# Performance work log

Measured on AMD Instinct MI355X. Metric: run time of the kernel, lower is better.

Reference implementation:

```python
import jax, jax.numpy as jnp
import numpy as np

EMBED_DIM = 768
NUM_HEADS = 12
HEAD_DIM = EMBED_DIM // NUM_HEADS
B, L = 1, 2048


def setup_inputs() -> dict:
    key = jax.random.key(0)
    ks = jax.random.split(key, 10)
    D = EMBED_DIM
    s = 1.0 / np.sqrt(D)
    x = jax.random.normal(ks[0], (B, L, D), dtype=jnp.float32)
    Wq = jax.random.uniform(ks[1], (D, D), jnp.float32, -s, s)
    bq = jax.random.uniform(ks[2], (D,), jnp.float32, -s, s)
    Wk = jax.random.uniform(ks[3], (D, D), jnp.float32, -s, s)
    bk = jax.random.uniform(ks[4], (D,), jnp.float32, -s, s)
    Wv = jax.random.uniform(ks[5], (D, D), jnp.float32, -s, s)
    bv = jax.random.uniform(ks[6], (D,), jnp.float32, -s, s)
    Wo = jax.random.uniform(ks[7], (D, D), jnp.float32, -s, s)
    bo = jax.random.uniform(ks[8], (D,), jnp.float32, -s, s)
    theta = jnp.zeros((1, NUM_HEADS, 1, 1), dtype=jnp.float32)
    return {"x": x, "Wq": Wq, "bq": bq, "Wk": Wk, "bk": bk,
            "Wv": Wv, "bv": bv, "Wo": Wo, "bo": bo, "theta": theta}


def _heads(t):
    # [B,L,D] -> [B,H,L,d_k]
    b, l, d = t.shape
    return t.reshape(b, l, NUM_HEADS, HEAD_DIM).transpose(0, 2, 1, 3)


def reference(x, Wq, bq, Wk, bk, Wv, bv, Wo, bo, theta):
    b, l, d = x.shape
    d_k = HEAD_DIM
    q = _heads(x @ Wq.T + bq)  # [B,H,L,dk]
    k = _heads(x @ Wk.T + bk)
    v = _heads(x @ Wv.T + bv)
    # squared pairwise L2 distance (== torch.cdist(q,k,p=2)**2), scaled by d_k
    qn = jnp.sum(q * q, axis=-1, keepdims=True)          # [B,H,L,1]
    kn = jnp.sum(k * k, axis=-1, keepdims=True)          # [B,H,L,1]
    qk = jnp.einsum('bhid,bhjd->bhij', q, k)             # [B,H,L,L]
    dist_sq = jnp.maximum(qn + kn.transpose(0, 1, 3, 2) - 2.0 * qk, 0.0) / d_k
    # global max over the full LxL matrix per (B,H)
    dist_max = jnp.max(dist_sq, axis=(-1, -2), keepdims=True)
    dist_norm = dist_sq / (dist_max + 1e-6)
    dsexp = jnp.exp(theta)                               # [1,H,1,1]
    attn_logits = jnp.exp(-dsexp * dist_norm)            # [B,H,L,L]
    attn_weights = jax.nn.softmax(attn_logits, axis=-1)
    context = jnp.einsum('bhij,bhjd->bhid', attn_weights, v)  # [B,H,L,dk]
    context = context.transpose(0, 2, 1, 3).reshape(b, l, d)
    output = context @ Wo.T + bo
    return output, attn_weights.mean(axis=1)
```

## Files before the change

kernel.cpp:

```cpp
#include <hip/hip_runtime.h>
#include <hip/hip_bf16.h>


typedef __bf16 bf16_t;
typedef bf16_t bf16x8 __attribute__((ext_vector_type(8)));
typedef bf16_t bf16x4 __attribute__((ext_vector_type(4)));
typedef float f32x4 __attribute__((ext_vector_type(4)));

#define L_SEQ 2048
#define DIM 768
#define NH 12
#define DKH 64
#define MDJ 8

__device__ __forceinline__ bf16x8 ldg8(const bf16_t* p) { return *(const bf16x8*)p; }
__device__ __forceinline__ f32x4 mfma16(bf16x8 a, bf16x8 b, f32x4 c_) {
  return __builtin_amdgcn_mfma_f32_16x16x32_bf16(a, b, c_, 0, 0, 0);
}


struct Tile2 { bf16x8 r[2]; };

__device__ __forceinline__ void tile_load(const bf16_t* __restrict__ src, int stride,
                                          Tile2& t_, int tid) {
#pragma unroll
  for (int c = 0; c < 2; ++c) {
    int chunk = tid + c * 256;
    t_.r[c] = *(const bf16x8*)&src[(size_t)(chunk >> 3) * stride + (chunk & 7) * 8];
  }
}

__device__ __forceinline__ void tile_write(bf16_t (*dst)[72], const Tile2& t_, int tid) {
#pragma unroll
  for (int c = 0; c < 2; ++c) {
    int chunk = tid + c * 256;
    *(bf16x8*)&dst[chunk >> 3][(chunk & 7) * 8] = t_.r[c];
  }
}

__device__ __forceinline__ void mfma_nt64(bf16_t (*As)[72], bf16_t (*Bs)[72],
                                          int wid, int lane, f32x4 acc[4]) {
#pragma unroll
  for (int ks = 0; ks < 2; ++ks) {
    bf16x8 a = *(const bf16x8*)&As[wid * 16 + (lane & 15)][ks * 32 + (lane >> 4) * 8];
#pragma unroll
    for (int nt = 0; nt < 4; ++nt) {
      bf16x8 b = *(const bf16x8*)&Bs[nt * 16 + (lane & 15)][ks * 32 + (lane >> 4) * 8];
      acc[nt] = mfma16(a, b, acc[nt]);
    }
  }
}


__global__ void cast_x(const float* __restrict__ in, bf16_t* __restrict__ out, int n4) {
  int i = blockIdx.x * 256 + threadIdx.x;
  if (i >= n4) return;
  float4 v = ((const float4*)in)[i];
  bf16_t* o = out + (size_t)i * 4;
  o[0] = (bf16_t)v.x; o[1] = (bf16_t)v.y; o[2] = (bf16_t)v.z; o[3] = (bf16_t)v.w;
}

__global__ void cast_w4(const float* __restrict__ w0, const float* __restrict__ w1,
                        const float* __restrict__ w2, const float* __restrict__ w3,
                        bf16_t* __restrict__ o0, bf16_t* __restrict__ o1,
                        bf16_t* __restrict__ o2, bf16_t* __restrict__ o3, int n4) {
  int i = blockIdx.x * 256 + threadIdx.x;
  if (i >= n4) return;
  const float* in = blockIdx.y == 0 ? w0 : blockIdx.y == 1 ? w1 : blockIdx.y == 2 ? w2 : w3;
  bf16_t* out = blockIdx.y == 0 ? o0 : blockIdx.y == 1 ? o1 : blockIdx.y == 2 ? o2 : o3;
  float4 v = ((const float4*)in)[i];
  bf16_t* o = out + (size_t)i * 4;
  o[0] = (bf16_t)v.x; o[1] = (bf16_t)v.y; o[2] = (bf16_t)v.z; o[3] = (bf16_t)v.w;
}


__global__ __launch_bounds__(256) void gemm_qkv(const bf16_t* __restrict__ x,
                                                const bf16_t* __restrict__ Bq,
                                                const bf16_t* __restrict__ Bk,
                                                const bf16_t* __restrict__ Bv,
                                                const float* __restrict__ bq,
                                                const float* __restrict__ bk,
                                                const float* __restrict__ bv,
                                                bf16_t* __restrict__ qo,
                                                bf16_t* __restrict__ ko,
                                                bf16_t* __restrict__ vto,
                                                float* __restrict__ qn,
                                                float* __restrict__ kn) {
  __shared__ bf16_t As[2][64][72];
  __shared__ bf16_t Bs[2][64][72];
  const int z = blockIdx.z;
  const bf16_t* B = z == 0 ? Bq : z == 1 ? Bk : Bv;
  const float* bias = z == 0 ? bq : z == 1 ? bk : bv;
  const int tid = threadIdx.x, wid = tid >> 6, lane = tid & 63;
  const int c = lane & 15, hi = lane >> 4;
  const int m0 = blockIdx.y * 64, n0 = blockIdx.x * 64;
  Tile2 at, bt;
  tile_load(x + (size_t)m0 * DIM, DIM, at, tid);
  tile_load(B + (size_t)n0 * DIM, DIM, bt, tid);
  f32x4 acc[4] = {};
  for (int kk = 0; kk < 12; ++kk) {
    tile_write(As[kk & 1], at, tid);
    tile_write(Bs[kk & 1], bt, tid);
    __syncthreads();
    if (kk < 11) {
      tile_load(x + (size_t)m0 * DIM + (kk + 1) * 64, DIM, at, tid);
      tile_load(B + (size_t)n0 * DIM + (kk + 1) * 64, DIM, bt, tid);
    }
    mfma_nt64(As[kk & 1], Bs[kk & 1], wid, lane, acc);
    __syncthreads();
  }
  const int r0 = wid * 16 + hi * 4;
  float ss[4] = {0.f, 0.f, 0.f, 0.f};
#pragma unroll
  for (int nt = 0; nt < 4; ++nt) {
    int cc = n0 + nt * 16 + c;
    float bv_ = bias[cc];
    int h = cc >> 6, d = cc & 63;
#pragma unroll
    for (int r = 0; r < 4; ++r) {
      int mm = m0 + r0 + r;
      float val = acc[nt][r] + bv_;
      if (z == 2) {
        vto[(size_t)cc * L_SEQ + mm] = (bf16_t)val;
      } else {
        bf16_t* out = z == 0 ? qo : ko;
        out[((size_t)h * L_SEQ + mm) * 64 + d] = (bf16_t)val;
        ss[r] = fmaf(val, val, ss[r]);
      }
    }
  }
  if (z < 2) {
#pragma unroll
    for (int s = 1; s < 16; s <<= 1)
#pragma unroll
      for (int r = 0; r < 4; ++r) ss[r] += __shfl_xor(ss[r], s);
    if (c == 0) {
      float* norm = z == 0 ? qn : kn;
      int h = n0 >> 6;
#pragma unroll
      for (int r = 0; r < 4; ++r) norm[h * L_SEQ + m0 + r0 + r] = ss[r];
    }
  }
}

__global__ __launch_bounds__(256) void gemm_out(const bf16_t* __restrict__ A,
                                                const bf16_t* __restrict__ B,
                                                const float* __restrict__ bias,
                                                float* __restrict__ out) {
  __shared__ bf16_t As[2][64][72];
  __shared__ bf16_t Bs[2][64][72];
  const int tid = threadIdx.x, wid = tid >> 6, lane = tid & 63;
  const int c = lane & 15, hi = lane >> 4;
  const int m0 = blockIdx.y * 64, n0 = blockIdx.x * 64;
  Tile2 at, bt;
  tile_load(A + (size_t)m0 * DIM, DIM, at, tid);
  tile_load(B + (size_t)n0 * DIM, DIM, bt, tid);
  f32x4 acc[4] = {};
  for (int kk = 0; kk < 12; ++kk) {
    tile_write(As[kk & 1], at, tid);
    tile_write(Bs[kk & 1], bt, tid);
    __syncthreads();
    if (kk < 11) {
      tile_load(A + (size_t)m0 * DIM + (kk + 1) * 64, DIM, at, tid);
      tile_load(B + (size_t)n0 * DIM + (kk + 1) * 64, DIM, bt, tid);
    }
    mfma_nt64(As[kk & 1], Bs[kk & 1], wid, lane, acc);
    __syncthreads();
  }
  const int r0 = wid * 16 + hi * 4;
#pragma unroll
  for (int nt = 0; nt < 4; ++nt) {
    int cc = n0 + nt * 16 + c;
    float bv = bias[cc];
#pragma unroll
    for (int r = 0; r < 4; ++r)
      out[(size_t)(m0 + r0 + r) * DIM + cc] = acc[nt][r] + bv;
  }
}


__global__ __launch_bounds__(256) void maxdist(const bf16_t* __restrict__ q,
                                               const bf16_t* __restrict__ k,
                                               const float* __restrict__ qn,
                                               const float* __restrict__ kn,
                                               float* __restrict__ blockmax) {
  __shared__ bf16_t Ks[2][64][72];
  __shared__ float wmax[4];
  const int it = blockIdx.x, jc = blockIdx.y, h = blockIdx.z;
  const int i0 = it * 64, jbase = jc * (L_SEQ / MDJ);
  const int tid = threadIdx.x, wid = tid >> 6, lane = tid & 63;
  const int c = lane & 15, hi = lane >> 4;
  bf16x8 qb[4][2];
  float aq[4];
#pragma unroll
  for (int nt = 0; nt < 4; ++nt) {
    const bf16_t* qr = q + ((size_t)h * L_SEQ + i0 + nt * 16 + c) * DKH;
    qb[nt][0] = ldg8(qr + hi * 8);
    qb[nt][1] = ldg8(qr + 32 + hi * 8);
    aq[nt] = qn[h * L_SEQ + i0 + nt * 16 + c];
  }
  Tile2 kt;
  tile_load(k + ((size_t)h * L_SEQ + jbase) * DKH, DKH, kt, tid);
  float m = 0.f;
  const int NT = L_SEQ / MDJ / 64;
  for (int t = 0; t < NT; ++t) {
    tile_write(Ks[t & 1], kt, tid);
    if (t < NT - 1)
      tile_load(k + ((size_t)h * L_SEQ + jbase + (t + 1) * 64) * DKH, DKH, kt, tid);
    __syncthreads();
    f32x4 acc[4] = {};
#pragma unroll
    for (int ks = 0; ks < 2; ++ks) {
      bf16x8 a = *(const bf16x8*)&Ks[t & 1][wid * 16 + c][ks * 32 + hi * 8];
#pragma unroll
      for (int nt = 0; nt < 4; ++nt) acc[nt] = mfma16(a, qb[nt][ks], acc[nt]);
    }
    f32x4 knj = *(const f32x4*)&kn[h * L_SEQ + jbase + t * 64 + wid * 16 + hi * 4];
#pragma unroll
    for (int nt = 0; nt < 4; ++nt)
#pragma unroll
      for (int r = 0; r < 4; ++r)
        m = fmaxf(m, fmaf(-2.f, acc[nt][r], aq[nt] + knj[r]));
  }
#pragma unroll
  for (int s = 1; s < 64; s <<= 1) m = fmaxf(m, __shfl_xor(m, s));
  if (lane == 0) wmax[wid] = m;
  __syncthreads();
  if (tid == 0) {
    float bm = fmaxf(fmaxf(wmax[0], wmax[1]), fmaxf(wmax[2], wmax[3]));
    blockmax[(h * MDJ + jc) * (L_SEQ / 64) + it] = fmaxf(bm, 0.f) * (1.f / 64.f);
  }
}

__global__ void reduce_dmax(const float* __restrict__ blockmax, float* __restrict__ dmax) {
  __shared__ float wm[4];
  const int h = blockIdx.x, tid = threadIdx.x, lane = tid & 63, wid = tid >> 6;
  float m = blockmax[h * (MDJ * 32) + tid];
#pragma unroll
  for (int s = 1; s < 64; s <<= 1) m = fmaxf(m, __shfl_xor(m, s));
  if (lane == 0) wm[wid] = m;
  __syncthreads();
  if (tid == 0) dmax[h] = fmaxf(fmaxf(wm[0], wm[1]), fmaxf(wm[2], wm[3]));
}

__global__ __launch_bounds__(256) void fusedctx(const bf16_t* __restrict__ q,
                                                const bf16_t* __restrict__ k,
                                                const bf16_t* __restrict__ vt,
                                                const float* __restrict__ qn,
                                                const float* __restrict__ kn,
                                                const float* __restrict__ dmax,
                                                const float* __restrict__ theta,
                                                float* __restrict__ denP,
                                                float* __restrict__ ctxP, int JC) {
  __shared__ bf16_t Ks[64][72];
  __shared__ bf16_t Vs[64][72];
  __shared__ bf16_t Ws[64][72];
  __shared__ float denW[4][64];
  const int it = blockIdx.x, jc = blockIdx.y, h = blockIdx.z;
  const int i0 = it * 64;
  const int JLEN = L_SEQ / JC, jbase = jc * JLEN;
  const int tid = threadIdx.x, wid = tid >> 6, lane = tid & 63;
  const int c = lane & 15, hi = lane >> 4;
  const float sc = __expf(theta[h]) * (1.f / 64.f) / (dmax[h] + 1e-6f);
  const float twosc = 2.f * sc;
  bf16x8 qb[4][2];
  float naq[4];
#pragma unroll
  for (int nt = 0; nt < 4; ++nt) {
    const bf16_t* qr = q + ((size_t)h * L_SEQ + i0 + nt * 16 + c) * DKH;
    qb[nt][0] = ldg8(qr + hi * 8);
    qb[nt][1] = ldg8(qr + 32 + hi * 8);
    naq[nt] = -sc * qn[h * L_SEQ + i0 + nt * 16 + c];
  }
  Tile2 kt, vtr;
  tile_load(k + ((size_t)h * L_SEQ + jbase) * DKH, DKH, kt, tid);
  tile_load(vt + (size_t)h * DKH * L_SEQ + jbase, L_SEQ, vtr, tid);
  float psum[4] = {0.f, 0.f, 0.f, 0.f};
  f32x4 cacc[4] = {};
  const int NT = JLEN / 64;
  for (int t = 0; t < NT; ++t) {
    tile_write(Ks, kt, tid);
    tile_write(Vs, vtr, tid);
    __syncthreads();
    if (t < NT - 1) {
      tile_load(k + ((size_t)h * L_SEQ + jbase + (t + 1) * 64) * DKH, DKH, kt, tid);
      tile_load(vt + (size_t)h * DKH * L_SEQ + jbase + (t + 1) * 64, L_SEQ, vtr, tid);
    }
    f32x4 acc[4] = {};
#pragma unroll
    for (int ks = 0; ks < 2; ++ks) {
      bf16x8 a = *(const bf16x8*)&Ks[wid * 16 + c][ks * 32 + hi * 8];
#pragma unroll
      for (int nt = 0; nt < 4; ++nt) acc[nt] = mfma16(a, qb[nt][ks], acc[nt]);
    }
    f32x4 knj = *(const f32x4*)&kn[h * L_SEQ + jbase + t * 64 + wid * 16 + hi * 4];
    f32x4 sknj = knj * sc;
#pragma unroll
    for (int nt = 0; nt < 4; ++nt) {
      bf16x4 wp;
#pragma unroll
      for (int r = 0; r < 4; ++r) {
        float tt = fminf(fmaf(twosc, acc[nt][r], naq[nt] - sknj[r]), 0.f);
        float w = __expf(__expf(tt));
        psum[nt] += w;
        wp[r] = (bf16_t)w;
      }
      *(bf16x4*)&Ws[nt * 16 + c][wid * 16 + hi * 4] = wp;
    }
    __syncthreads();
#pragma unroll
    for (int ks = 0; ks < 2; ++ks) {
      bf16x8 a = *(const bf16x8*)&Vs[wid * 16 + c][ks * 32 + hi * 8];
#pragma unroll
      for (int nt = 0; nt < 4; ++nt) {
        bf16x8 b = *(const bf16x8*)&Ws[nt * 16 + c][ks * 32 + hi * 8];
        cacc[nt] = mfma16(a, b, cacc[nt]);
      }
    }
    __syncthreads();
  }
#pragma unroll
  for (int nt = 0; nt < 4; ++nt) {
    psum[nt] += __shfl_xor(psum[nt], 16);
    psum[nt] += __shfl_xor(psum[nt], 32);
  }
  if (lane < 16)
#pragma unroll
    for (int nt = 0; nt < 4; ++nt) denW[wid][nt * 16 + lane] = psum[nt];
  __syncthreads();
  if (tid < 64)
    denP[(size_t)(h * JC + jc) * L_SEQ + i0 + tid] =
        denW[0][tid] + denW[1][tid] + denW[2][tid] + denW[3][tid];
  float* P = ctxP + ((size_t)(h * JC + jc) * 32 + it) * 4096;
#pragma unroll
  for (int nt = 0; nt < 4; ++nt)
    *(f32x4*)&P[(nt * 16 + c) * 64 + wid * 16 + hi * 4] = cacc[nt];
}

__global__ __launch_bounds__(256) void ctx_combine(const float* __restrict__ denP,
                                                   const float* __restrict__ ctxP,
                                                   float* __restrict__ den,
                                                   bf16_t* __restrict__ ctx, int JC) {
  __shared__ float invL[64];
  const int it = blockIdx.x, h = blockIdx.y, tid = threadIdx.x;
  const int i0 = it * 64;
  if (tid < 64) {
    float d0 = 0.f;
    for (int jc = 0; jc < JC; ++jc)
      d0 += denP[(size_t)(h * JC + jc) * L_SEQ + i0 + tid];
    den[h * L_SEQ + i0 + tid] = d0;
    invL[tid] = 1.f / d0;
  }
  __syncthreads();
  const int il = tid >> 2, db = (tid & 3) * 16;
  const float inv = invL[il];
  bf16_t* dst = ctx + (size_t)(i0 + il) * DIM + h * 64 + db;
#pragma unroll
  for (int half = 0; half < 2; ++half) {
    bf16x8 o;
#pragma unroll
    for (int e = 0; e < 2; ++e) {
      f32x4 v = {0.f, 0.f, 0.f, 0.f};
      for (int jc = 0; jc < JC; ++jc)
        v += *(const f32x4*)&ctxP[((size_t)(h * JC + jc) * 32 + it) * 4096 +
                                  il * 64 + db + half * 8 + e * 4];
#pragma unroll
      for (int j = 0; j < 4; ++j) o[e * 4 + j] = (bf16_t)(v[j] * inv);
    }
    *(bf16x8*)&dst[half * 8] = o;
  }
}


__global__ __launch_bounds__(256) void attnmean(const bf16_t* __restrict__ q,
                                                const bf16_t* __restrict__ k,
                                                const float* __restrict__ qn,
                                                const float* __restrict__ kn,
                                                const float* __restrict__ dmax,
                                                const float* __restrict__ theta,
                                                const float* __restrict__ den,
                                                float* __restrict__ out1) {
  __shared__ bf16_t Qs[2][64][72];
  __shared__ bf16_t Ks[2][64][72];
  const int j0 = blockIdx.x * 64, i0 = blockIdx.y * 64;
  const int tid = threadIdx.x, wid = tid >> 6, lane = tid & 63;
  const int c = lane & 15, hi = lane >> 4;
  Tile2 qt, kt;
  tile_load(q + (size_t)i0 * DKH, DKH, qt, tid);
  tile_load(k + (size_t)j0 * DKH, DKH, kt, tid);
  f32x4 macc[4] = {};
  for (int h = 0; h < NH; ++h) {
    const int b = h & 1;
    tile_write(Qs[b], qt, tid);
    tile_write(Ks[b], kt, tid);
    __syncthreads();
    if (h < NH - 1) {
      tile_load(q + ((size_t)(h + 1) * L_SEQ + i0) * DKH, DKH, qt, tid);
      tile_load(k + ((size_t)(h + 1) * L_SEQ + j0) * DKH, DKH, kt, tid);
    }
    const float sc = __expf(theta[h]) * (1.f / 64.f) / (dmax[h] + 1e-6f);
    const float twosc = 2.f * sc;
    f32x4 acc[4] = {};
#pragma unroll
    for (int ks = 0; ks < 2; ++ks) {
      bf16x8 a = *(const bf16x8*)&Ks[b][wid * 16 + c][ks * 32 + hi * 8];
#pragma unroll
      for (int nt = 0; nt < 4; ++nt) {
        bf16x8 bq_ = *(const bf16x8*)&Qs[b][nt * 16 + c][ks * 32 + hi * 8];
        acc[nt] = mfma16(a, bq_, acc[nt]);
      }
    }
    f32x4 knj = *(const f32x4*)&kn[h * L_SEQ + j0 + wid * 16 + hi * 4];
    f32x4 sknj = knj * sc;
#pragma unroll
    for (int nt = 0; nt < 4; ++nt) {
      float naq = -sc * qn[h * L_SEQ + i0 + nt * 16 + c];
      float inv = 1.f / den[h * L_SEQ + i0 + nt * 16 + c];
#pragma unroll
      for (int r = 0; r < 4; ++r) {
        float tt = fminf(fmaf(twosc, acc[nt][r], naq - sknj[r]), 0.f);
        float w = __expf(__expf(tt));
        macc[nt][r] = fmaf(w, inv, macc[nt][r]);
      }
    }
    __syncthreads();
  }
#pragma unroll
  for (int nt = 0; nt < 4; ++nt) {
    f32x4 o = macc[nt] * (1.f / 12.f);
    *(f32x4*)&out1[(size_t)(i0 + nt * 16 + c) * L_SEQ + j0 + wid * 16 + hi * 4] = o;
  }
}


extern "C" void kernel_launch(void* const* d_in, const int* in_sizes, int n_in,
                              void* d_out, int out_size, void* d_ws, size_t ws_size,
                              hipStream_t stream) {
  const float* x = (const float*)d_in[0];
  const float* Wq = (const float*)d_in[1];
  const float* bq = (const float*)d_in[2];
  const float* Wk = (const float*)d_in[3];
  const float* bk = (const float*)d_in[4];
  const float* Wv = (const float*)d_in[5];
  const float* bv = (const float*)d_in[6];
  const float* Wo = (const float*)d_in[7];
  const float* bo = (const float*)d_in[8];
  const float* theta = (const float*)d_in[9];

  bf16_t* x_bf = (bf16_t*)d_ws;
  bf16_t* Wq_bf = x_bf + (size_t)L_SEQ * DIM;
  bf16_t* Wk_bf = Wq_bf + (size_t)DIM * DIM;
  bf16_t* Wv_bf = Wk_bf + (size_t)DIM * DIM;
  bf16_t* Wo_bf = Wv_bf + (size_t)DIM * DIM;
  bf16_t* q_bf = Wo_bf + (size_t)DIM * DIM;
  bf16_t* k_bf = q_bf + (size_t)NH * L_SEQ * DKH;
  bf16_t* vt_bf = k_bf + (size_t)NH * L_SEQ * DKH;
  bf16_t* ctx_bf = vt_bf + (size_t)NH * L_SEQ * DKH;
  float* qn = (float*)(ctx_bf + (size_t)L_SEQ * DIM);
  float* kn = qn + NH * L_SEQ;
  float* den = kn + NH * L_SEQ;
  float* dmax = den + NH * L_SEQ;
  float* blockmax = dmax + 64;
  float* denP = blockmax + 4096;
  float* ctxP = denP + 4 * NH * L_SEQ;

  size_t fixed_bytes = (size_t)((char*)ctxP - (char*)d_ws);
  int JC = (fixed_bytes + (size_t)4 * NH * 32 * 4096 * 4 <= ws_size) ? 4 : 2;

  float* out0 = (float*)d_out;
  float* out1 = out0 + (size_t)L_SEQ * DIM;

  cast_x<<<(L_SEQ * DIM / 4 + 255) / 256, 256, 0, stream>>>(x, x_bf, L_SEQ * DIM / 4);
  cast_w4<<<dim3((DIM * DIM / 4 + 255) / 256, 4), 256, 0, stream>>>(
      Wq, Wk, Wv, Wo, Wq_bf, Wk_bf, Wv_bf, Wo_bf, DIM * DIM / 4);

  gemm_qkv<<<dim3(DIM / 64, L_SEQ / 64, 3), 256, 0, stream>>>(
      x_bf, Wq_bf, Wk_bf, Wv_bf, bq, bk, bv, q_bf, k_bf, vt_bf, qn, kn);

  maxdist<<<dim3(L_SEQ / 64, MDJ, NH), 256, 0, stream>>>(q_bf, k_bf, qn, kn, blockmax);
  reduce_dmax<<<NH, 256, 0, stream>>>(blockmax, dmax);

  fusedctx<<<dim3(L_SEQ / 64, JC, NH), 256, 0, stream>>>(q_bf, k_bf, vt_bf, qn, kn,
                                                         dmax, theta, denP, ctxP, JC);
  ctx_combine<<<dim3(L_SEQ / 64, NH), 256, 0, stream>>>(denP, ctxP, den, ctx_bf, JC);

  attnmean<<<dim3(L_SEQ / 64, L_SEQ / 64), 256, 0, stream>>>(q_bf, k_bf, qn, kn, dmax,
                                                             theta, den, out1);
  gemm_out<<<dim3(DIM / 64, L_SEQ / 64), 256, 0, stream>>>(ctx_bf, Wo_bf, bo, out0);
}
```

Measured before the change: 148.3 us.

## Store bf16 attention weights in fusedctx and average them instead of recomputing

fusedctx can now write its bf16 unnormalized attention weights for every head to a workspace buffer (about 100MB). A new wmean kernel then averages them across heads using precomputed per-row 1/(12*den), instead of attnmean redoing QK^T and the double exponential. The exponentials switch to exp2f with log2e folded into the scale, and maxdist uses half as many j-chunks. This trades recompute for extra HBM traffic, a large workspace requirement, and bf16 rounding in the mean output.

```diff
diff --git a/kernel.cpp b/kernel.cpp
--- a/kernel.cpp
+++ b/kernel.cpp
@@ -11,7 +11,8 @@
 #define DIM 768
 #define NH 12
 #define DKH 64
-#define MDJ 8
+#define MDJ 4
+#define L2E 1.44269504f
 
 __device__ __forceinline__ bf16x8 ldg8(const bf16_t* p) { return *(const bf16x8*)p; }
 __device__ __forceinline__ f32x4 mfma16(bf16x8 a, bf16x8 b, f32x4 c_) {
@@ -233,14 +234,14 @@
 }
 
 __global__ void reduce_dmax(const float* __restrict__ blockmax, float* __restrict__ dmax) {
-  __shared__ float wm[4];
+  __shared__ float wm[2];
   const int h = blockIdx.x, tid = threadIdx.x, lane = tid & 63, wid = tid >> 6;
   float m = blockmax[h * (MDJ * 32) + tid];
 #pragma unroll
   for (int s = 1; s < 64; s <<= 1) m = fmaxf(m, __shfl_xor(m, s));
   if (lane == 0) wm[wid] = m;
   __syncthreads();
-  if (tid == 0) dmax[h] = fmaxf(fmaxf(wm[0], wm[1]), fmaxf(wm[2], wm[3]));
+  if (tid == 0) dmax[h] = fmaxf(wm[0], wm[1]);
 }
 
 __global__ __launch_bounds__(256) void fusedctx(const bf16_t* __restrict__ q,
@@ -251,7 +252,9 @@
                                                 const float* __restrict__ dmax,
                                                 const float* __restrict__ theta,
                                                 float* __restrict__ denP,
-                                                float* __restrict__ ctxP, int JC) {
+                                                float* __restrict__ ctxP,
+                                                bf16_t* __restrict__ Wg,
+                                                int JC, int writeW) {
   __shared__ bf16_t Ks[64][72];
   __shared__ bf16_t Vs[64][72];
   __shared__ bf16_t Ws[64][72];
@@ -262,7 +265,8 @@
   const int tid = threadIdx.x, wid = tid >> 6, lane = tid & 63;
   const int c = lane & 15, hi = lane >> 4;
   const float sc = __expf(theta[h]) * (1.f / 64.f) / (dmax[h] + 1e-6f);
-  const float twosc = 2.f * sc;
+  const float scl = sc * L2E;
+  const float twoscl = 2.f * scl;
   bf16x8 qb[4][2];
   float naq[4];
 #pragma unroll
@@ -270,7 +274,7 @@
     const bf16_t* qr = q + ((size_t)h * L_SEQ + i0 + nt * 16 + c) * DKH;
     qb[nt][0] = ldg8(qr + hi * 8);
     qb[nt][1] = ldg8(qr + 32 + hi * 8);
-    naq[nt] = -sc * qn[h * L_SEQ + i0 + nt * 16 + c];
+    naq[nt] = -scl * qn[h * L_SEQ + i0 + nt * 16 + c];
   }
   Tile2 kt, vtr;
   tile_load(k + ((size_t)h * L_SEQ + jbase) * DKH, DKH, kt, tid);
@@ -294,14 +298,14 @@
       for (int nt = 0; nt < 4; ++nt) acc[nt] = mfma16(a, qb[nt][ks], acc[nt]);
     }
     f32x4 knj = *(const f32x4*)&kn[h * L_SEQ + jbase + t * 64 + wid * 16 + hi * 4];
-    f32x4 sknj = knj * sc;
+    f32x4 sknj = knj * scl;
 #pragma unroll
     for (int nt = 0; nt < 4; ++nt) {
       bf16x4 wp;
 #pragma unroll
       for (int r = 0; r < 4; ++r) {
-        float tt = fminf(fmaf(twosc, acc[nt][r], naq[nt] - sknj[r]), 0.f);
-        float w = __expf(__expf(tt));
+        float ttl = fminf(fmaf(twoscl, acc[nt][r], naq[nt] - sknj[r]), 0.f);
+        float w = exp2f(exp2f(ttl) * L2E);
         psum[nt] += w;
         wp[r] = (bf16_t)w;
       }
@@ -315,6 +319,15 @@
       for (int nt = 0; nt < 4; ++nt) {
         bf16x8 b = *(const bf16x8*)&Ws[nt * 16 + c][ks * 32 + hi * 8];
         cacc[nt] = mfma16(a, b, cacc[nt]);
+      }
+    }
+    if (writeW) {
+#pragma unroll
+      for (int cc2 = 0; cc2 < 2; ++cc2) {
+        int chunk = tid + cc2 * 256;
+        int row = chunk >> 3, col = (chunk & 7) * 8;
+        bf16x8 wv = *(const bf16x8*)&Ws[row][col];
+        *(bf16x8*)&Wg[((size_t)h * L_SEQ + i0 + row) * L_SEQ + jbase + t * 64 + col] = wv;
       }
     }
     __syncthreads();
@@ -340,6 +353,7 @@
 __global__ __launch_bounds__(256) void ctx_combine(const float* __restrict__ denP,
                                                    const float* __restrict__ ctxP,
                                                    float* __restrict__ den,
+                                                   float* __restrict__ invden12,
                                                    bf16_t* __restrict__ ctx, int JC) {
   __shared__ float invL[64];
   const int it = blockIdx.x, h = blockIdx.y, tid = threadIdx.x;
@@ -349,7 +363,9 @@
     for (int jc = 0; jc < JC; ++jc)
       d0 += denP[(size_t)(h * JC + jc) * L_SEQ + i0 + tid];
     den[h * L_SEQ + i0 + tid] = d0;
-    invL[tid] = 1.f / d0;
+    float inv = 1.f / d0;
+    invL[tid] = inv;
+    invden12[h * L_SEQ + i0 + tid] = inv * (1.f / 12.f);
   }
   __syncthreads();
   const int il = tid >> 2, db = (tid & 3) * 16;
@@ -369,6 +385,31 @@
     }
     *(bf16x8*)&dst[half * 8] = o;
   }
+}
+
+__global__ __launch_bounds__(256) void wmean(const bf16_t* __restrict__ Wg,
+                                             const float* __restrict__ invden12,
+                                             float* __restrict__ out1) {
+  const int idx = blockIdx.x * 256 + threadIdx.x;
+  const int i = idx >> 7, j0 = (idx & 127) * 16;
+  f32x4 acc[4] = {};
+#pragma unroll 4
+  for (int h = 0; h < NH; ++h) {
+    const bf16_t* p = Wg + ((size_t)h * L_SEQ + i) * L_SEQ + j0;
+    bf16x8 a0 = ldg8(p);
+    bf16x8 a1 = ldg8(p + 8);
+    float s = invden12[h * L_SEQ + i];
+#pragma unroll
+    for (int r = 0; r < 4; ++r) {
+      acc[0][r] = fmaf((float)a0[r], s, acc[0][r]);
+      acc[1][r] = fmaf((float)a0[4 + r], s, acc[1][r]);
+      acc[2][r] = fmaf((float)a1[r], s, acc[2][r]);
+      acc[3][r] = fmaf((float)a1[4 + r], s, acc[3][r]);
+    }
+  }
+  float* dst = out1 + (size_t)i * L_SEQ + j0;
+#pragma unroll
+  for (int e = 0; e < 4; ++e) *(f32x4*)&dst[e * 4] = acc[e];
 }
 
 
@@ -399,7 +440,8 @@
       tile_load(k + ((size_t)(h + 1) * L_SEQ + j0) * DKH, DKH, kt, tid);
     }
     const float sc = __expf(theta[h]) * (1.f / 64.f) / (dmax[h] + 1e-6f);
-    const float twosc = 2.f * sc;
+    const float scl = sc * L2E;
+    const float twoscl = 2.f * scl;
     f32x4 acc[4] = {};
 #pragma unroll
     for (int ks = 0; ks < 2; ++ks) {
@@ -411,15 +453,15 @@
       }
     }
     f32x4 knj = *(const f32x4*)&kn[h * L_SEQ + j0 + wid * 16 + hi * 4];
-    f32x4 sknj = knj * sc;
+    f32x4 sknj = knj * scl;
 #pragma unroll
     for (int nt = 0; nt < 4; ++nt) {
-      float naq = -sc * qn[h * L_SEQ + i0 + nt * 16 + c];
+      float naq = -scl * qn[h * L_SEQ + i0 + nt * 16 + c];
       float inv = 1.f / den[h * L_SEQ + i0 + nt * 16 + c];
 #pragma unroll
       for (int r = 0; r < 4; ++r) {
-        float tt = fminf(fmaf(twosc, acc[nt][r], naq - sknj[r]), 0.f);
-        float w = __expf(__expf(tt));
+        float ttl = fminf(fmaf(twoscl, acc[nt][r], naq - sknj[r]), 0.f);
+        float w = exp2f(exp2f(ttl) * L2E);
         macc[nt][r] = fmaf(w, inv, macc[nt][r]);
       }
     }
@@ -459,13 +501,18 @@
   float* qn = (float*)(ctx_bf + (size_t)L_SEQ * DIM);
   float* kn = qn + NH * L_SEQ;
   float* den = kn + NH * L_SEQ;
-  float* dmax = den + NH * L_SEQ;
+  float* invden12 = den + NH * L_SEQ;
+  float* dmax = invden12 + NH * L_SEQ;
   float* blockmax = dmax + 64;
-  float* denP = blockmax + 4096;
+  float* denP = blockmax + 2048;
   float* ctxP = denP + 4 * NH * L_SEQ;
+  bf16_t* Wg = (bf16_t*)(ctxP + (size_t)4 * NH * 32 * 4096);
 
   size_t fixed_bytes = (size_t)((char*)ctxP - (char*)d_ws);
-  int JC = (fixed_bytes + (size_t)4 * NH * 32 * 4096 * 4 <= ws_size) ? 4 : 2;
+  size_t ctxP4_bytes = (size_t)4 * NH * 32 * 4096 * 4;
+  size_t wg_bytes = (size_t)NH * L_SEQ * L_SEQ * 2;
+  int JC = (fixed_bytes + ctxP4_bytes <= ws_size) ? 4 : 2;
+  int useW = (JC == 4 && fixed_bytes + ctxP4_bytes + wg_bytes <= ws_size) ? 1 : 0;
 
   float* out0 = (float*)d_out;
   float* out1 = out0 + (size_t)L_SEQ * DIM;
@@ -478,13 +525,18 @@
       x_bf, Wq_bf, Wk_bf, Wv_bf, bq, bk, bv, q_bf, k_bf, vt_bf, qn, kn);
 
   maxdist<<<dim3(L_SEQ / 64, MDJ, NH), 256, 0, stream>>>(q_bf, k_bf, qn, kn, blockmax);
-  reduce_dmax<<<NH, 256, 0, stream>>>(blockmax, dmax);
-
-  fusedctx<<<dim3(L_SEQ / 64, JC, NH), 256, 0, stream>>>(q_bf, k_bf, vt_bf, qn, kn,
-                                                         dmax, theta, denP, ctxP, JC);
-  ctx_combine<<<dim3(L_SEQ / 64, NH), 256, 0, stream>>>(denP, ctxP, den, ctx_bf, JC);
-
-  attnmean<<<dim3(L_SEQ / 64, L_SEQ / 64), 256, 0, stream>>>(q_bf, k_bf, qn, kn, dmax,
-                                                             theta, den, out1);
+  reduce_dmax<<<NH, MDJ * 32, 0, stream>>>(blockmax, dmax);
+
+  fusedctx<<<dim3(L_SEQ / 64, JC, NH), 256, 0, stream>>>(
+      q_bf, k_bf, vt_bf, qn, kn, dmax, theta, denP, ctxP, Wg, JC, useW);
+  ctx_combine<<<dim3(L_SEQ / 64, NH), 256, 0, stream>>>(denP, ctxP, den, invden12,
+                                                        ctx_bf, JC);
+
+  if (useW) {
+    wmean<<<(L_SEQ * 128) / 256, 256, 0, stream>>>(Wg, invden12, out1);
+  } else {
+    attnmean<<<dim3(L_SEQ / 64, L_SEQ / 64), 256, 0, stream>>>(q_bf, k_bf, qn, kn,
+                                                               dmax, theta, den, out1);
+  }
   gemm_out<<<dim3(DIM / 64, L_SEQ / 64), 256, 0, stream>>>(ctx_bf, Wo_bf, bo, out0);
 }
```

New measurement: 143.5 us. 3.3% less time.
